# Kernel optimization log

Hardware: AMD Instinct MI355X
Metric: run time of the kernel (lower is better)

Reference implementation:

```python
import jax, jax.numpy as jnp
import numpy as np

N = 50000          # nodes
E = 800000         # edges (before self-loops)
IN_C = 128         # input feature dim
H = 4              # attention heads
C = 32             # channels per head (hidden == out == 32)
G = 64             # graphs in the batch
NEG_SLOPE_ATT = 0.2   # PyG GATConv default negative_slope
NEG_SLOPE_ACT = 0.01  # nn.LeakyReLU default


def setup_inputs() -> dict:
    key = jax.random.key(0)
    ks = jax.random.split(key, 16)
    x = jax.random.normal(ks[0], (N, IN_C), dtype=jnp.float32)
    edge_index = jax.random.randint(ks[1], (2, E), 0, N, dtype=jnp.int64)
    batch = jnp.sort(jax.random.randint(ks[2], (N,), 0, G, dtype=jnp.int64))
    def gat_params(k, din):
        k1, k2, k3 = jax.random.split(k, 3)
        W = jax.random.normal(k1, (din, H * C), dtype=jnp.float32) * (1.0 / np.sqrt(din))
        a_src = jax.random.normal(k2, (H, C), dtype=jnp.float32) * 0.1
        a_dst = jax.random.normal(k3, (H, C), dtype=jnp.float32) * 0.1
        b = jnp.zeros((H * C,), dtype=jnp.float32)
        return W, a_src, a_dst, b
    W1, a_src1, a_dst1, b1 = gat_params(ks[3], IN_C)
    W2, a_src2, a_dst2, b2 = gat_params(ks[4], H * C)
    W3, a_src3, a_dst3, b3 = gat_params(ks[5], H * C)
    return dict(x=x, edge_index=edge_index, batch=batch,
                W1=W1, a_src1=a_src1, a_dst1=a_dst1, b1=b1,
                W2=W2, a_src2=a_src2, a_dst2=a_dst2, b2=b2,
                W3=W3, a_src3=a_src3, a_dst3=a_dst3, b3=b3)


def _gat_conv(x, src, dst, W, a_src, a_dst, b):
    """PyG GATConv (concat=True, negative_slope=0.2); self-loops already in src/dst."""
    n = x.shape[0]
    h = (x @ W).reshape(n, H, C)                      # [N,H,C]
    s = jnp.einsum('nhc,hc->nh', h, a_src)            # [N,H]
    d = jnp.einsum('nhc,hc->nh', h, a_dst)            # [N,H]
    e = jax.nn.leaky_relu(s[src] + d[dst], NEG_SLOPE_ATT)  # [E',H]
    # segment softmax over incoming edges of each destination node
    m = jax.ops.segment_max(e, dst, num_segments=n)   # [N,H]
    ex = jnp.exp(e - m[dst])
    denom = jax.ops.segment_sum(ex, dst, num_segments=n)
    alpha = ex / denom[dst]                           # [E',H]
    msg = h[src] * alpha[..., None]                   # [E',H,C]
    out = jax.ops.segment_sum(msg, dst, num_segments=n).reshape(n, H * C)
    return out + b


def reference(x, edge_index, batch,
              W1, a_src1, a_dst1, b1,
              W2, a_src2, a_dst2, b2,
              W3, a_src3, a_dst3, b3):
    n = x.shape[0]
    # add self-loops (PyG GATConv default add_self_loops=True)
    loop = jnp.arange(n, dtype=edge_index.dtype)
    src = jnp.concatenate([edge_index[0], loop])
    dst = jnp.concatenate([edge_index[1], loop])
    # dropout is identity in eval mode
    h = jax.nn.leaky_relu(_gat_conv(x, src, dst, W1, a_src1, a_dst1, b1), NEG_SLOPE_ACT)
    h = jax.nn.leaky_relu(_gat_conv(h, src, dst, W2, a_src2, a_dst2, b2), NEG_SLOPE_ACT)
    h = jax.nn.leaky_relu(_gat_conv(h, src, dst, W3, a_src3, a_dst3, b3), NEG_SLOPE_ACT)
    graph_embedding = jax.ops.segment_max(h, batch, num_segments=G)  # [G, H*C]
    return (graph_embedding, h, edge_index)
```

## Files before the change

kernel.cpp:

```cpp
#include <hip/hip_runtime.h>
#include <math.h>
#include <limits.h>

#define LRELU_ATT 0.2f
#define LRELU_ACT 0.01f
#define CAP 64
#define DPB 16
#define LCAP (DPB * CAP)
#define NBMAX 512
#define TILE 8192
#define BCAP 6528

__device__ __forceinline__ float lrelu(float x, float s) { return x > 0.f ? x : x * s; }

__device__ __forceinline__ void atomicMaxF(float* addr, float val) {
    int* ai = (int*)addr;
    int old = *(volatile int*)ai;
    while (__int_as_float(old) < val) {
        int assumed = old;
        old = atomicCAS(ai, assumed, __float_as_int(val));
        if (old == assumed) break;
    }
}

__device__ __forceinline__ unsigned short f2bf(float f) {
    union { float f; unsigned u; } v; v.f = f;
    unsigned r = v.u + 0x7FFF + ((v.u >> 16) & 1);
    return (unsigned short)(r >> 16);
}
__device__ __forceinline__ float bflo(unsigned u) {
    union { unsigned u; float f; } v; v.u = u << 16;
    return v.f;
}
__device__ __forceinline__ float bfhi(unsigned u) {
    union { unsigned u; float f; } v; v.u = u & 0xffff0000u;
    return v.f;
}

__device__ __forceinline__ int* scan_incl_512(int* a, int* b, int tid, int nthr) {
    int* in = a; int* out = b;
    for (int off = 1; off < 512; off <<= 1) {
        for (int i = tid; i < 512; i += nthr)
            out[i] = in[i] + (i >= off ? in[i - off] : 0);
        __syncthreads();
        int* t = in; in = out; out = t;
    }
    return in;
}

__global__ __launch_bounds__(256) void gemm_k(const float* __restrict__ X,
                                              const float* __restrict__ Wm,
                                              const float* __restrict__ a_src,
                                              const float* __restrict__ a_dst,
                                              unsigned short* __restrict__ Hb,
                                              float* __restrict__ S,
                                              float* __restrict__ D, int n) {
    __shared__ float sW[32 * 128];
    __shared__ float sX[32 * 32];
    __shared__ float sa[128], sb[128];
    if (threadIdx.x < 128) {
        sa[threadIdx.x] = a_src[threadIdx.x];
        sb[threadIdx.x] = a_dst[threadIdx.x];
    }
    int row0 = blockIdx.x * 32;
    int rt = threadIdx.x >> 5;
    int ct = threadIdx.x & 31;
    int c0 = ct * 4;
    float4 acc[4];
#pragma unroll
    for (int i = 0; i < 4; i++) acc[i] = make_float4(0.f, 0.f, 0.f, 0.f);

    for (int k0 = 0; k0 < 128; k0 += 32) {
        __syncthreads();
        for (int i = threadIdx.x * 4; i < 32 * 128; i += 1024)
            *(float4*)&sW[i] = *(const float4*)&Wm[(k0 + (i >> 7)) * 128 + (i & 127)];
        {
            int i = threadIdx.x * 4;
            int r = i >> 5, kk = i & 31;
            int gr = row0 + r;
            float4 v = make_float4(0.f, 0.f, 0.f, 0.f);
            if (gr < n) v = *(const float4*)&X[gr * 128 + k0 + kk];
            *(float4*)&sX[i] = v;
        }
        __syncthreads();
#pragma unroll
        for (int kk = 0; kk < 32; kk += 4) {
            float4 w0 = *(const float4*)&sW[(kk + 0) * 128 + c0];
            float4 w1 = *(const float4*)&sW[(kk + 1) * 128 + c0];
            float4 w2 = *(const float4*)&sW[(kk + 2) * 128 + c0];
            float4 w3 = *(const float4*)&sW[(kk + 3) * 128 + c0];
#pragma unroll
            for (int i = 0; i < 4; i++) {
                float4 xv = *(const float4*)&sX[(rt * 4 + i) * 32 + kk];
                acc[i].x = fmaf(xv.x, w0.x, acc[i].x);
                acc[i].y = fmaf(xv.x, w0.y, acc[i].y);
                acc[i].z = fmaf(xv.x, w0.z, acc[i].z);
                acc[i].w = fmaf(xv.x, w0.w, acc[i].w);
                acc[i].x = fmaf(xv.y, w1.x, acc[i].x);
                acc[i].y = fmaf(xv.y, w1.y, acc[i].y);
                acc[i].z = fmaf(xv.y, w1.z, acc[i].z);
                acc[i].w = fmaf(xv.y, w1.w, acc[i].w);
                acc[i].x = fmaf(xv.z, w2.x, acc[i].x);
                acc[i].y = fmaf(xv.z, w2.y, acc[i].y);
                acc[i].z = fmaf(xv.z, w2.z, acc[i].z);
                acc[i].w = fmaf(xv.z, w2.w, acc[i].w);
                acc[i].x = fmaf(xv.w, w3.x, acc[i].x);
                acc[i].y = fmaf(xv.w, w3.y, acc[i].y);
                acc[i].z = fmaf(xv.w, w3.z, acc[i].z);
                acc[i].w = fmaf(xv.w, w3.w, acc[i].w);
            }
        }
    }
    float sp[4], dp[4];
    const float* ap = &sa[c0];
    const float* bp = &sb[c0];
#pragma unroll
    for (int i = 0; i < 4; i++) {
        sp[i] = acc[i].x * ap[0] + acc[i].y * ap[1] + acc[i].z * ap[2] + acc[i].w * ap[3];
        dp[i] = acc[i].x * bp[0] + acc[i].y * bp[1] + acc[i].z * bp[2] + acc[i].w * bp[3];
    }
#pragma unroll
    for (int o = 1; o < 8; o <<= 1) {
#pragma unroll
        for (int i = 0; i < 4; i++) {
            sp[i] += __shfl_xor(sp[i], o, 64);
            dp[i] += __shfl_xor(dp[i], o, 64);
        }
    }
    int hd = ct >> 3;
#pragma unroll
    for (int i = 0; i < 4; i++) {
        int gr = row0 + rt * 4 + i;
        if (gr < n) {
            ushort4 hb;
            hb.x = f2bf(acc[i].x); hb.y = f2bf(acc[i].y);
            hb.z = f2bf(acc[i].z); hb.w = f2bf(acc[i].w);
            *(ushort4*)&Hb[gr * 128 + c0] = hb;
            if ((ct & 7) == 0) {
                S[gr * 4 + hd] = sp[i];
                D[gr * 4 + hd] = dp[i];
            }
        }
    }
}

__global__ void fill_f_k(float* __restrict__ p, float v, int cnt) {
    int i = blockIdx.x * blockDim.x + threadIdx.x;
    if (i < cnt) p[i] = v;
}
__global__ void fill_i_k(int* __restrict__ p, int v, int cnt) {
    int i = blockIdx.x * blockDim.x + threadIdx.x;
    if (i < cnt) p[i] = v;
}


__global__ void bhist_k(const int* __restrict__ ei, int* __restrict__ bcount, int E) {
    __shared__ int h[NBMAX];
    for (int i = threadIdx.x; i < NBMAX; i += 256) h[i] = 0;
    __syncthreads();
    for (int e = blockIdx.x * blockDim.x + threadIdx.x; e < E; e += gridDim.x * blockDim.x)
        atomicAdd(&h[ei[E + e] >> 7], 1);
    __syncthreads();
    for (int i = threadIdx.x; i < NBMAX; i += 256)
        if (h[i]) atomicAdd(&bcount[i], h[i]);
}

__global__ void bscan_k(const int* __restrict__ bcount, int* __restrict__ bbase,
                        int* __restrict__ cursor, int NB) {
    __shared__ int sa[512], sb[512];
    int tid = threadIdx.x;
    for (int i = tid; i < 512; i += 256) sa[i] = (i < NB) ? bcount[i] : 0;
    __syncthreads();
    int* inc = scan_incl_512(sa, sb, tid, 256);
    for (int i = tid; i < NB; i += 256) {
        int ex = i ? inc[i - 1] : 0;
        bbase[i] = ex;
        cursor[i] = ex;
    }
    if (tid == 0) bbase[NB] = inc[NB - 1];
}

__global__ __launch_bounds__(256) void bin_scatter_k(const int* __restrict__ ei,
                                                     int* __restrict__ cursor,
                                                     unsigned* __restrict__ binned, int E) {
    __shared__ int hist[NBMAX], excl[NBMAX], curl[NBMAX], gbase[NBMAX];
    __shared__ int sa[512], sb[512];
    __shared__ unsigned staged[TILE];
    int tid = threadIdx.x;
    int e0 = blockIdx.x * TILE;
    for (int i = tid; i < NBMAX; i += 256) hist[i] = 0;
    __syncthreads();
    unsigned keys[TILE / 256];
#pragma unroll
    for (int j = 0; j < TILE / 256; j++) {
        int e = e0 + j * 256 + tid;
        if (e < E) {
            unsigned dst = (unsigned)ei[E + e];
            unsigned src = (unsigned)ei[e];
            unsigned k = (dst << 16) | src;
            keys[j] = k;
            atomicAdd(&hist[k >> 23], 1);
        } else keys[j] = 0xFFFFFFFFu;
    }
    __syncthreads();
    for (int i = tid; i < 512; i += 256) sa[i] = hist[i];
    __syncthreads();
    int* inc = scan_incl_512(sa, sb, tid, 256);
    for (int i = tid; i < NBMAX; i += 256) {
        int ex = i ? inc[i - 1] : 0;
        excl[i] = ex;
        curl[i] = ex;
    }
    __syncthreads();
#pragma unroll
    for (int j = 0; j < TILE / 256; j++) {
        unsigned k = keys[j];
        if (k != 0xFFFFFFFFu) {
            int b = k >> 23;
            int p = atomicAdd(&curl[b], 1);
            staged[p] = k;
        }
    }
    __syncthreads();
    for (int i = tid; i < NBMAX; i += 256) {
        int cnt = hist[i];
        if (cnt) gbase[i] = atomicAdd(&cursor[i], cnt);
    }
    __syncthreads();
    int total = inc[511];
    for (int p = tid; p < total; p += 256) {
        unsigned k = staged[p];
        int b = k >> 23;
        binned[gbase[b] + (p - excl[b])] = k;
    }
}

__global__ __launch_bounds__(1024) void bucket_csr_k(const unsigned* __restrict__ binned,
                                                     const int* __restrict__ bbase,
                                                     int* __restrict__ rowptr,
                                                     int* __restrict__ csr,
                                                     int n, int NB) {
    __shared__ int outL[BCAP];
    __shared__ int sa[512], sb[512];
    __shared__ int lbase[129], cur[128];
    int b = blockIdx.x;
    int tid = threadIdx.x;
    int dst0 = b << 7;
    int ndst = min(128, n - dst0);
    int ebase = bbase[b], ecnt = bbase[b + 1] - ebase;
    for (int i = tid; i < 512; i += 1024) sa[i] = (i < ndst) ? 1 : 0;
    __syncthreads();
    for (int p = tid; p < ecnt; p += 1024) {
        int ld = (int)(binned[ebase + p] >> 16) - dst0;
        atomicAdd(&sa[ld], 1);
    }
    __syncthreads();
    int* inc = scan_incl_512(sa, sb, tid, 1024);
    for (int i = tid; i < ndst; i += 1024) {
        int ex = i ? inc[i - 1] : 0;
        lbase[i] = ex;
        cur[i] = ex;
    }
    if (tid == 0) lbase[ndst] = inc[ndst - 1];
    __syncthreads();
    int total = lbase[ndst];
    for (int i = tid; i < ndst; i += 1024) {
        int p = atomicAdd(&cur[i], 1);
        outL[p] = dst0 + i;
    }
    for (int p = tid; p < ecnt; p += 1024) {
        unsigned k = binned[ebase + p];
        int ld = (int)(k >> 16) - dst0;
        int pos = atomicAdd(&cur[ld], 1);
        outL[pos] = (int)(k & 0xFFFFu);
    }
    __syncthreads();
    int w = tid >> 6, lane = tid & 63;
    for (int d = w; d < ndst; d += 16) {
        int st = lbase[d], en = lbase[d + 1];
        int deg = en - st;
        if (deg <= 1) continue;
        if (deg <= 64) {
            int v = (lane < deg) ? outL[st + lane] : INT_MAX;
            int r = 0;
            for (int j = 0; j < deg; j++) {
                int kj = __shfl(v, j, 64);
                r += (kj < v) || (kj == v && j < lane);
            }
            if (lane < deg) outL[st + r] = v;
        } else if (deg <= 128) {
            int v0 = (lane < deg) ? outL[st + lane] : 0;
            int v1 = (64 + lane < deg) ? outL[st + 64 + lane] : 0;
            int r0 = 0, r1 = 0;
            for (int j = 0; j < deg; j++) {
                int kj = outL[st + j];
                r0 += (kj < v0) || (kj == v0 && j < lane);
                r1 += (kj < v1) || (kj == v1 && j < 64 + lane);
            }
            if (lane < deg) outL[st + r0] = v0;
            if (64 + lane < deg) outL[st + r1] = v1;
        } else if (lane == 0) {
            for (int q = st + 1; q < en; q++) {
                int key = outL[q];
                int r = q - 1;
                while (r >= st && outL[r] > key) { outL[r + 1] = outL[r]; r--; }
                outL[r + 1] = key;
            }
        }
    }
    __syncthreads();
    int gb = ebase + dst0;
    for (int p = tid; p < total; p += 1024) csr[gb + p] = outL[p];
    for (int i = tid; i < ndst; i += 1024) rowptr[dst0 + i] = gb + lbase[i];
    if (b == NB - 1 && tid == 0) rowptr[n] = gb + total;
}

__global__ __launch_bounds__(256) void attn_agg_k(const int* __restrict__ rowptr,
                                                  const int* __restrict__ csr,
                                                  const float* __restrict__ S,
                                                  const float* __restrict__ Dv,
                                                  const unsigned short* __restrict__ Hb,
                                                  const float* __restrict__ bias,
                                                  float* __restrict__ Out, int n) {
    __shared__ float al[DPB][CAP * 4];
    __shared__ int srcs[LCAP];
    __shared__ float sm[DPB][4], srd[DPB][4], sdv[DPB][4];
    __shared__ int srp[DPB + 1];
    int tid = threadIdx.x;
    int base = blockIdx.x * DPB;
    if (tid <= DPB) {
        int idx = base + tid;
        srp[tid] = rowptr[idx > n ? n : idx];
    }
    __syncthreads();
    int st0 = srp[0];
    int etot = srp[DPB] - st0;
    for (int i = tid; i < etot && i < LCAP; i += 256) srcs[i] = csr[st0 + i];
    __syncthreads();

    {
        int g = tid >> 4;
        int l = tid & 15;
        int dst = base + g;
        if (dst < n) {
            int lst = srp[g] - st0;
            int deg = srp[g + 1] - srp[g];
            float4 dv = *(const float4*)&Dv[dst * 4];
            float4 m = make_float4(-INFINITY, -INFINITY, -INFINITY, -INFINITY);
            for (int pos = l; pos < deg; pos += 16) {
                int idx = lst + pos;
                int src = (idx < LCAP) ? srcs[idx] : csr[st0 + idx];
                float4 sv = *(const float4*)&S[src * 4];
                float4 e;
                e.x = lrelu(sv.x + dv.x, LRELU_ATT);
                e.y = lrelu(sv.y + dv.y, LRELU_ATT);
                e.z = lrelu(sv.z + dv.z, LRELU_ATT);
                e.w = lrelu(sv.w + dv.w, LRELU_ATT);
                if (pos < CAP) *(float4*)&al[g][pos * 4] = e;
                m.x = fmaxf(m.x, e.x); m.y = fmaxf(m.y, e.y);
                m.z = fmaxf(m.z, e.z); m.w = fmaxf(m.w, e.w);
            }
#pragma unroll
            for (int o = 1; o < 16; o <<= 1) {
                m.x = fmaxf(m.x, __shfl_xor(m.x, o, 64));
                m.y = fmaxf(m.y, __shfl_xor(m.y, o, 64));
                m.z = fmaxf(m.z, __shfl_xor(m.z, o, 64));
                m.w = fmaxf(m.w, __shfl_xor(m.w, o, 64));
            }
            float4 den = make_float4(0.f, 0.f, 0.f, 0.f);
            for (int pos = l; pos < deg; pos += 16) {
                float4 e;
                if (pos < CAP) e = *(const float4*)&al[g][pos * 4];
                else {
                    int idx = lst + pos;
                    int src = (idx < LCAP) ? srcs[idx] : csr[st0 + idx];
                    float4 sv = *(const float4*)&S[src * 4];
                    e.x = lrelu(sv.x + dv.x, LRELU_ATT);
                    e.y = lrelu(sv.y + dv.y, LRELU_ATT);
                    e.z = lrelu(sv.z + dv.z, LRELU_ATT);
                    e.w = lrelu(sv.w + dv.w, LRELU_ATT);
                }
                float4 ex;
                ex.x = __expf(e.x - m.x); ex.y = __expf(e.y - m.y);
                ex.z = __expf(e.z - m.z); ex.w = __expf(e.w - m.w);
                den.x += ex.x; den.y += ex.y; den.z += ex.z; den.w += ex.w;
                if (pos < CAP) *(float4*)&al[g][pos * 4] = ex;
            }
#pragma unroll
            for (int o = 1; o < 16; o <<= 1) {
                den.x += __shfl_xor(den.x, o, 64);
                den.y += __shfl_xor(den.y, o, 64);
                den.z += __shfl_xor(den.z, o, 64);
                den.w += __shfl_xor(den.w, o, 64);
            }
            float4 rd;
            rd.x = 1.f / den.x; rd.y = 1.f / den.y;
            rd.z = 1.f / den.z; rd.w = 1.f / den.w;
            int lim = deg < CAP ? deg : CAP;
            for (int pos = l; pos < lim; pos += 16) {
                float4 ex = *(const float4*)&al[g][pos * 4];
                ex.x *= rd.x; ex.y *= rd.y; ex.z *= rd.z; ex.w *= rd.w;
                *(float4*)&al[g][pos * 4] = ex;
            }
            if (l == 0) {
                *(float4*)&sm[g][0] = m;
                *(float4*)&srd[g][0] = rd;
                *(float4*)&sdv[g][0] = dv;
            }
        }
    }
    __syncthreads();

    int w = tid >> 6;
    int lane = tid & 63;
    int slot = lane >> 4;
    int l16 = lane & 15;
    int ch0 = l16 * 8;
    int hd = l16 >> 2;
#pragma unroll
    for (int j = 0; j < 4; j++) {
        int g2 = w * 4 + j;
        int dst = base + g2;
        if (dst >= n) break;
        int lst = srp[g2] - st0;
        int deg = srp[g2 + 1] - srp[g2];
        float4 a0 = make_float4(0.f, 0.f, 0.f, 0.f);
        float4 a1 = make_float4(0.f, 0.f, 0.f, 0.f);
        float4 b0 = make_float4(0.f, 0.f, 0.f, 0.f);
        float4 b1 = make_float4(0.f, 0.f, 0.f, 0.f);
        int pos = slot;
        for (; pos + 4 < deg; pos += 8) {
            int iA = lst + pos, iB = iA + 4;
            int srcA = (iA < LCAP) ? srcs[iA] : csr[st0 + iA];
            int srcB = (iB < LCAP) ? srcs[iB] : csr[st0 + iB];
            float aA = (pos < CAP) ? al[g2][pos * 4 + hd]
                : __expf(lrelu(S[srcA * 4 + hd] + sdv[g2][hd], LRELU_ATT) - sm[g2][hd]) * srd[g2][hd];
            float aB = (pos + 4 < CAP) ? al[g2][(pos + 4) * 4 + hd]
                : __expf(lrelu(S[srcB * 4 + hd] + sdv[g2][hd], LRELU_ATT) - sm[g2][hd]) * srd[g2][hd];
            uint4 hvA = *(const uint4*)&Hb[srcA * 128 + ch0];
            uint4 hvB = *(const uint4*)&Hb[srcB * 128 + ch0];
            a0.x = fmaf(aA, bflo(hvA.x), a0.x);
            a0.y = fmaf(aA, bfhi(hvA.x), a0.y);
            a0.z = fmaf(aA, bflo(hvA.y), a0.z);
            a0.w = fmaf(aA, bfhi(hvA.y), a0.w);
            a1.x = fmaf(aA, bflo(hvA.z), a1.x);
            a1.y = fmaf(aA, bfhi(hvA.z), a1.y);
            a1.z = fmaf(aA, bflo(hvA.w), a1.z);
            a1.w = fmaf(aA, bfhi(hvA.w), a1.w);
            b0.x = fmaf(aB, bflo(hvB.x), b0.x);
            b0.y = fmaf(aB, bfhi(hvB.x), b0.y);
            b0.z = fmaf(aB, bflo(hvB.y), b0.z);
            b0.w = fmaf(aB, bfhi(hvB.y), b0.w);
            b1.x = fmaf(aB, bflo(hvB.z), b1.x);
            b1.y = fmaf(aB, bfhi(hvB.z), b1.y);
            b1.z = fmaf(aB, bflo(hvB.w), b1.z);
            b1.w = fmaf(aB, bfhi(hvB.w), b1.w);
        }
        if (pos < deg) {
            int iA = lst + pos;
            int srcA = (iA < LCAP) ? srcs[iA] : csr[st0 + iA];
            float aA = (pos < CAP) ? al[g2][pos * 4 + hd]
                : __expf(lrelu(S[srcA * 4 + hd] + sdv[g2][hd], LRELU_ATT) - sm[g2][hd]) * srd[g2][hd];
            uint4 hvA = *(const uint4*)&Hb[srcA * 128 + ch0];
            a0.x = fmaf(aA, bflo(hvA.x), a0.x);
            a0.y = fmaf(aA, bfhi(hvA.x), a0.y);
            a0.z = fmaf(aA, bflo(hvA.y), a0.z);
            a0.w = fmaf(aA, bfhi(hvA.y), a0.w);
            a1.x = fmaf(aA, bflo(hvA.z), a1.x);
            a1.y = fmaf(aA, bfhi(hvA.z), a1.y);
            a1.z = fmaf(aA, bflo(hvA.w), a1.z);
            a1.w = fmaf(aA, bfhi(hvA.w), a1.w);
        }
        a0.x += b0.x; a0.y += b0.y; a0.z += b0.z; a0.w += b0.w;
        a1.x += b1.x; a1.y += b1.y; a1.z += b1.z; a1.w += b1.w;
#pragma unroll
        for (int o = 16; o <= 32; o <<= 1) {
            a0.x += __shfl_xor(a0.x, o, 64);
            a0.y += __shfl_xor(a0.y, o, 64);
            a0.z += __shfl_xor(a0.z, o, 64);
            a0.w += __shfl_xor(a0.w, o, 64);
            a1.x += __shfl_xor(a1.x, o, 64);
            a1.y += __shfl_xor(a1.y, o, 64);
            a1.z += __shfl_xor(a1.z, o, 64);
            a1.w += __shfl_xor(a1.w, o, 64);
        }
        if (slot == 0) {
            float4 c0v = *(const float4*)&bias[ch0];
            float4 c1v = *(const float4*)&bias[ch0 + 4];
            float4 o0, o1;
            o0.x = lrelu(a0.x + c0v.x, LRELU_ACT);
            o0.y = lrelu(a0.y + c0v.y, LRELU_ACT);
            o0.z = lrelu(a0.z + c0v.z, LRELU_ACT);
            o0.w = lrelu(a0.w + c0v.w, LRELU_ACT);
            o1.x = lrelu(a1.x + c1v.x, LRELU_ACT);
            o1.y = lrelu(a1.y + c1v.y, LRELU_ACT);
            o1.z = lrelu(a1.z + c1v.z, LRELU_ACT);
            o1.w = lrelu(a1.w + c1v.w, LRELU_ACT);
            *(float4*)&Out[dst * 128 + ch0] = o0;
            *(float4*)&Out[dst * 128 + ch0 + 4] = o1;
        }
    }
}

__global__ void ge_max_k(const float* __restrict__ Hf, const int* __restrict__ batch,
                         float* __restrict__ ge, int n) {
    int c = threadIdx.x & 127;
    int rh = threadIdx.x >> 7;
    int node0 = blockIdx.x * 128;
    int hi = min(node0 + 128, n);
    int gid = -1;
    float mv = -INFINITY;
    for (int r = node0 + rh; r < hi; r += 2) {
        int g = batch[r];
        if (g != gid) {
            if (gid >= 0) atomicMaxF(&ge[gid * 128 + c], mv);
            gid = g;
            mv = -INFINITY;
        }
        mv = fmaxf(mv, Hf[r * 128 + c]);
    }
    if (gid >= 0) atomicMaxF(&ge[gid * 128 + c], mv);
}

__global__ void ei_copy_k(const int* __restrict__ ei, float* __restrict__ out, int m) {
    int i = (blockIdx.x * blockDim.x + threadIdx.x) * 4;
    if (i + 3 < m) {
        int4 v = *(const int4*)&ei[i];
        float4 o = make_float4((float)v.x, (float)v.y, (float)v.z, (float)v.w);
        *(float4*)&out[i] = o;
    } else {
        for (; i < m; i++) out[i] = (float)ei[i];
    }
}

extern "C" void kernel_launch(void* const* d_in, const int* in_sizes, int n_in,
                              void* d_out, int out_size, void* d_ws, size_t ws_size,
                              hipStream_t stream) {
    const float* x = (const float*)d_in[0];
    const int* ei = (const int*)d_in[1];
    const int* batch = (const int*)d_in[2];
    const float* Wm[3]   = {(const float*)d_in[3], (const float*)d_in[7],  (const float*)d_in[11]};
    const float* asrc[3] = {(const float*)d_in[4], (const float*)d_in[8],  (const float*)d_in[12]};
    const float* adst[3] = {(const float*)d_in[5], (const float*)d_in[9],  (const float*)d_in[13]};
    const float* bias[3] = {(const float*)d_in[6], (const float*)d_in[10], (const float*)d_in[14]};

    const int n = in_sizes[2];
    const int E = in_sizes[1] / 2;
    const int ne = E + n;
    const int G = (out_size - n * 128 - 2 * E) / 128;
    const int NB = (n + 127) >> 7;

    char* w = (char*)d_ws;
    float* Xact = (float*)w;          w += (size_t)n * 128 * 4;
    unsigned short* Hb = (unsigned short*)w; w += (size_t)n * 128 * 2;
    float* S    = (float*)w; w += (size_t)n * 4 * 4;
    float* D    = (float*)w; w += (size_t)n * 4 * 4;
    int* bcount = (int*)w;   w += NBMAX * 4;
    int* bbase  = (int*)w;   w += (NBMAX + 1) * 4;
    int* cursor = (int*)w;   w += NBMAX * 4;
    int* rowptr = (int*)w;   w += (size_t)(n + 1) * 4;
    unsigned* binned = (unsigned*)w; w += (size_t)E * 4;
    int* csr    = (int*)w;   w += (size_t)ne * 4;

    float* out   = (float*)d_out;
    float* ge    = out;
    float* hout  = out + (size_t)G * 128;
    float* eiout = out + (size_t)G * 128 + (size_t)n * 128;

    fill_i_k<<<(NBMAX + 255) / 256, 256, 0, stream>>>(bcount, 0, NBMAX);
    bhist_k<<<256, 256, 0, stream>>>(ei, bcount, E);
    bscan_k<<<1, 256, 0, stream>>>(bcount, bbase, cursor, NB);
    bin_scatter_k<<<(E + TILE - 1) / TILE, 256, 0, stream>>>(ei, cursor, binned, E);
    bucket_csr_k<<<NB, 1024, 0, stream>>>(binned, bbase, rowptr, csr, n, NB);

    const float* xin = x;
    for (int L = 0; L < 3; L++) {
        gemm_k<<<(n + 31) / 32, 256, 0, stream>>>(xin, Wm[L], asrc[L], adst[L], Hb, S, D, n);
        float* xnext = (L == 2) ? hout : Xact;
        attn_agg_k<<<(n + DPB - 1) / DPB, 256, 0, stream>>>(rowptr, csr, S, D, Hb, bias[L], xnext, n);
        xin = xnext;
    }

    fill_f_k<<<(G * 128 + 255) / 256, 256, 0, stream>>>(ge, -INFINITY, G * 128);
    ge_max_k<<<(n + 127) / 128, 256, 0, stream>>>(hout, batch, ge, n);
    ei_copy_k<<<(2 * E / 4 + 255) / 256, 256, 0, stream>>>(ei, eiout, 2 * E);
}
```

Baseline: 321.1 us.

## Rewrite node projection GEMM to use bf16 MFMA with transposed LDS tiles

Replaces the fp32 FMA register-tiled GEMM with a bf16 MFMA (16x16x32) kernel. Each block now handles 64 rows, converts X and W to bf16 into padded, transposed shared-memory tiles, and folds the attention dot products into the MFMA output layout with wider shuffle reductions. The aim is to cut the time spent on the per-layer N×128×128 projection. The trade-off is reduced GEMM input precision, since inputs were fp32 before. Each block also reloads and converts the full 128×128 weight matrix.

```diff
diff --git a/kernel.cpp b/kernel.cpp
--- a/kernel.cpp
+++ b/kernel.cpp
@@ -10,6 +10,10 @@
 #define NBMAX 512
 #define TILE 8192
 #define BCAP 6528
+#define WPAD 136
+
+typedef __attribute__((ext_vector_type(8))) short bf16x8;
+typedef __attribute__((ext_vector_type(4))) float f32x4;
 
 __device__ __forceinline__ float lrelu(float x, float s) { return x > 0.f ? x : x * s; }
 
@@ -55,90 +59,83 @@
                                               unsigned short* __restrict__ Hb,
                                               float* __restrict__ S,
                                               float* __restrict__ D, int n) {
-    __shared__ float sW[32 * 128];
-    __shared__ float sX[32 * 32];
+    __shared__ unsigned short sWt[128 * WPAD];
+    __shared__ unsigned short sXt[64 * WPAD];
     __shared__ float sa[128], sb[128];
-    if (threadIdx.x < 128) {
-        sa[threadIdx.x] = a_src[threadIdx.x];
-        sb[threadIdx.x] = a_dst[threadIdx.x];
-    }
-    int row0 = blockIdx.x * 32;
-    int rt = threadIdx.x >> 5;
-    int ct = threadIdx.x & 31;
-    int c0 = ct * 4;
-    float4 acc[4];
-#pragma unroll
-    for (int i = 0; i < 4; i++) acc[i] = make_float4(0.f, 0.f, 0.f, 0.f);
-
-    for (int k0 = 0; k0 < 128; k0 += 32) {
-        __syncthreads();
-        for (int i = threadIdx.x * 4; i < 32 * 128; i += 1024)
-            *(float4*)&sW[i] = *(const float4*)&Wm[(k0 + (i >> 7)) * 128 + (i & 127)];
-        {
-            int i = threadIdx.x * 4;
-            int r = i >> 5, kk = i & 31;
-            int gr = row0 + r;
-            float4 v = make_float4(0.f, 0.f, 0.f, 0.f);
-            if (gr < n) v = *(const float4*)&X[gr * 128 + k0 + kk];
-            *(float4*)&sX[i] = v;
-        }
-        __syncthreads();
-#pragma unroll
-        for (int kk = 0; kk < 32; kk += 4) {
-            float4 w0 = *(const float4*)&sW[(kk + 0) * 128 + c0];
-            float4 w1 = *(const float4*)&sW[(kk + 1) * 128 + c0];
-            float4 w2 = *(const float4*)&sW[(kk + 2) * 128 + c0];
-            float4 w3 = *(const float4*)&sW[(kk + 3) * 128 + c0];
-#pragma unroll
-            for (int i = 0; i < 4; i++) {
-                float4 xv = *(const float4*)&sX[(rt * 4 + i) * 32 + kk];
-                acc[i].x = fmaf(xv.x, w0.x, acc[i].x);
-                acc[i].y = fmaf(xv.x, w0.y, acc[i].y);
-                acc[i].z = fmaf(xv.x, w0.z, acc[i].z);
-                acc[i].w = fmaf(xv.x, w0.w, acc[i].w);
-                acc[i].x = fmaf(xv.y, w1.x, acc[i].x);
-                acc[i].y = fmaf(xv.y, w1.y, acc[i].y);
-                acc[i].z = fmaf(xv.y, w1.z, acc[i].z);
-                acc[i].w = fmaf(xv.y, w1.w, acc[i].w);
-                acc[i].x = fmaf(xv.z, w2.x, acc[i].x);
-                acc[i].y = fmaf(xv.z, w2.y, acc[i].y);
-                acc[i].z = fmaf(xv.z, w2.z, acc[i].z);
-                acc[i].w = fmaf(xv.z, w2.w, acc[i].w);
-                acc[i].x = fmaf(xv.w, w3.x, acc[i].x);
-                acc[i].y = fmaf(xv.w, w3.y, acc[i].y);
-                acc[i].z = fmaf(xv.w, w3.z, acc[i].z);
-                acc[i].w = fmaf(xv.w, w3.w, acc[i].w);
-            }
-        }
-    }
-    float sp[4], dp[4];
-    const float* ap = &sa[c0];
-    const float* bp = &sb[c0];
-#pragma unroll
-    for (int i = 0; i < 4; i++) {
-        sp[i] = acc[i].x * ap[0] + acc[i].y * ap[1] + acc[i].z * ap[2] + acc[i].w * ap[3];
-        dp[i] = acc[i].x * bp[0] + acc[i].y * bp[1] + acc[i].z * bp[2] + acc[i].w * bp[3];
-    }
-#pragma unroll
-    for (int o = 1; o < 8; o <<= 1) {
-#pragma unroll
-        for (int i = 0; i < 4; i++) {
-            sp[i] += __shfl_xor(sp[i], o, 64);
-            dp[i] += __shfl_xor(dp[i], o, 64);
-        }
-    }
-    int hd = ct >> 3;
-#pragma unroll
-    for (int i = 0; i < 4; i++) {
-        int gr = row0 + rt * 4 + i;
+    int tid = threadIdx.x;
+    if (tid < 128) { sa[tid] = a_src[tid]; sb[tid] = a_dst[tid]; }
+    int row0 = blockIdx.x * 64;
+#pragma unroll
+    for (int i = 0; i < 16; i++) {
+        int idx4 = tid + 256 * i;
+        int k = idx4 >> 5;
+        int n0 = (idx4 & 31) * 4;
+        float4 wv = *(const float4*)&Wm[k * 128 + n0];
+        sWt[(n0 + 0) * WPAD + k] = f2bf(wv.x);
+        sWt[(n0 + 1) * WPAD + k] = f2bf(wv.y);
+        sWt[(n0 + 2) * WPAD + k] = f2bf(wv.z);
+        sWt[(n0 + 3) * WPAD + k] = f2bf(wv.w);
+    }
+#pragma unroll
+    for (int i = 0; i < 8; i++) {
+        int idx4 = tid + 256 * i;
+        int r = idx4 >> 5;
+        int koff = (idx4 & 31) * 4;
+        int gr = row0 + r;
+        float4 xv = make_float4(0.f, 0.f, 0.f, 0.f);
+        if (gr < n) xv = *(const float4*)&X[gr * 128 + koff];
+        ushort4 xb;
+        xb.x = f2bf(xv.x); xb.y = f2bf(xv.y); xb.z = f2bf(xv.z); xb.w = f2bf(xv.w);
+        *(ushort4*)&sXt[r * WPAD + koff] = xb;
+    }
+    __syncthreads();
+    int w = tid >> 6, l = tid & 63;
+    int lr = l & 15, lk = l >> 4;
+    f32x4 acc[8];
+#pragma unroll
+    for (int ct = 0; ct < 8; ct++) acc[ct] = (f32x4){0.f, 0.f, 0.f, 0.f};
+#pragma unroll
+    for (int ks = 0; ks < 4; ks++) {
+        int kbase = ks * 32 + lk * 8;
+        bf16x8 afrag = *(const bf16x8*)&sXt[(w * 16 + lr) * WPAD + kbase];
+#pragma unroll
+        for (int ct = 0; ct < 8; ct++) {
+            bf16x8 bfrag = *(const bf16x8*)&sWt[(ct * 16 + lr) * WPAD + kbase];
+            acc[ct] = __builtin_amdgcn_mfma_f32_16x16x32_bf16(afrag, bfrag, acc[ct], 0, 0, 0);
+        }
+    }
+    float sp[4][4], dp[4][4];
+#pragma unroll
+    for (int reg = 0; reg < 4; reg++) {
+#pragma unroll
+        for (int hd = 0; hd < 4; hd++) {
+            int c0 = (2 * hd) * 16 + lr;
+            int c1 = (2 * hd + 1) * 16 + lr;
+            sp[reg][hd] = acc[2 * hd][reg] * sa[c0] + acc[2 * hd + 1][reg] * sa[c1];
+            dp[reg][hd] = acc[2 * hd][reg] * sb[c0] + acc[2 * hd + 1][reg] * sb[c1];
+        }
+    }
+#pragma unroll
+    for (int o = 1; o < 16; o <<= 1) {
+#pragma unroll
+        for (int reg = 0; reg < 4; reg++) {
+#pragma unroll
+            for (int hd = 0; hd < 4; hd++) {
+                sp[reg][hd] += __shfl_xor(sp[reg][hd], o, 64);
+                dp[reg][hd] += __shfl_xor(dp[reg][hd], o, 64);
+            }
+        }
+    }
+#pragma unroll
+    for (int reg = 0; reg < 4; reg++) {
+        int gr = row0 + w * 16 + lk * 4 + reg;
         if (gr < n) {
-            ushort4 hb;
-            hb.x = f2bf(acc[i].x); hb.y = f2bf(acc[i].y);
-            hb.z = f2bf(acc[i].z); hb.w = f2bf(acc[i].w);
-            *(ushort4*)&Hb[gr * 128 + c0] = hb;
-            if ((ct & 7) == 0) {
-                S[gr * 4 + hd] = sp[i];
-                D[gr * 4 + hd] = dp[i];
+#pragma unroll
+            for (int ct = 0; ct < 8; ct++)
+                Hb[gr * 128 + ct * 16 + lr] = f2bf(acc[ct][reg]);
+            if (lr == 0) {
+                *(float4*)&S[gr * 4] = make_float4(sp[reg][0], sp[reg][1], sp[reg][2], sp[reg][3]);
+                *(float4*)&D[gr * 4] = make_float4(dp[reg][0], dp[reg][1], dp[reg][2], dp[reg][3]);
             }
         }
     }
@@ -152,7 +149,6 @@
     int i = blockIdx.x * blockDim.x + threadIdx.x;
     if (i < cnt) p[i] = v;
 }
-
 
 __global__ void bhist_k(const int* __restrict__ ei, int* __restrict__ bcount, int E) {
     __shared__ int h[NBMAX];
@@ -575,7 +571,7 @@
 
     const float* xin = x;
     for (int L = 0; L < 3; L++) {
-        gemm_k<<<(n + 31) / 32, 256, 0, stream>>>(xin, Wm[L], asrc[L], adst[L], Hb, S, D, n);
+        gemm_k<<<(n + 63) / 64, 256, 0, stream>>>(xin, Wm[L], asrc[L], adst[L], Hb, S, D, n);
         float* xnext = (L == 2) ? hout : Xact;
         attn_agg_k<<<(n + DPB - 1) / DPB, 256, 0, stream>>>(rowptr, csr, S, D, Hb, bias[L], xnext, n);
         xin = xnext;
```

New measurement: 308.5 us. -3.9%, faster.
